# Performance work log

Measured on AMD Instinct MI355X. Metric: run time of the kernel, lower is better.

The kernel has to match this reference:

```python
import jax, jax.numpy as jnp
import numpy as np

B, N, L, D = 4, 32, 64, 512      # batch, num_nodes, his_len, input_dim
H, O = 1024, 512                  # expert hidden, output_dim
E, S, TOP_K = 16, 3, 2            # independent experts, shared experts, top-k


def setup_inputs() -> dict:
    key = jax.random.key(0)
    ks = jax.random.split(key, 12)
    sc = 0.02
    return {
        "feature_vectors": jax.random.normal(ks[0], (B, N, L, D), jnp.float32),
        "object_types": jax.random.uniform(ks[1], (B, N, L, S, 1), jnp.float32),
        "gating_w": jax.random.normal(ks[2], (D, E), jnp.float32) * sc,
        "gating_b": jnp.zeros((E,), jnp.float32),
        "sh_w1": jax.random.normal(ks[3], (S, D, H), jnp.float32) * sc,
        "sh_b1": jnp.zeros((S, H), jnp.float32),
        "sh_w2": jax.random.normal(ks[4], (S, H, O), jnp.float32) * sc,
        "sh_b2": jnp.zeros((S, O), jnp.float32),
        "ind_w1": jax.random.normal(ks[5], (E, D, H), jnp.float32) * sc,
        "ind_b1": jnp.zeros((E, H), jnp.float32),
        "ind_w2": jax.random.normal(ks[6], (E, H, O), jnp.float32) * sc,
        "ind_b2": jnp.zeros((E, O), jnp.float32),
    }


def reference(feature_vectors, object_types, gating_w, gating_b,
              sh_w1, sh_b1, sh_w2, sh_b2,
              ind_w1, ind_b1, ind_w2, ind_b2):
    b, n, l, d = feature_vectors.shape
    x = feature_vectors.reshape(-1, d)                       # [T, D]
    T = x.shape[0]

    # gating: softmax -> top-k -> renormalize selected weights
    gating = jax.nn.softmax(x @ gating_w + gating_b, axis=-1)  # [T, E]
    vals, idx = jax.lax.top_k(gating, TOP_K)                   # [T, K]
    w = vals / vals.sum(axis=-1, keepdims=True)                # [T, K]

    # shared experts: per-type FFN, weighted by object_types
    obj = object_types.reshape(-1, S, 1)                       # [T, S, 1]
    sh_h = jax.nn.relu(jnp.einsum('td,sdh->tsh', x, sh_w1) + sh_b1)
    sh_o = jnp.einsum('tsh,sho->tso', sh_h, sh_w2) + sh_b2     # [T, S, O]
    shared_out = (sh_o * obj).sum(axis=1)                      # [T, O]

    # independent experts: dense all-expert compute, combine via top-k weights
    # (equivalent to the bincount/mask dispatch loop: unselected experts get 0)
    ind_h = jax.nn.relu(jnp.einsum('td,edh->teh', x, ind_w1) + ind_b1)
    ind_o = jnp.einsum('teh,eho->teo', ind_h, ind_w2) + ind_b2  # [T, E, O]
    comb = jnp.zeros((T, gating_w.shape[1]), x.dtype)
    comb = comb.at[jnp.arange(T)[:, None], idx].add(w)          # [T, E] sparse weights
    ind_out = jnp.einsum('te,teo->to', comb, ind_o)             # [T, O]

    out = 0.5 * shared_out + 0.5 * ind_out
    return out.reshape(b, n, l, -1)
```

## Files before the change

kernel.cpp:

```cpp
#include <hip/hip_runtime.h>
#include <hip/hip_bf16.h>
#include <stdint.h>

#define T_TOK 8192
#define DIM   512
#define HID   1024
#define ODIM  512
#define NEXP  16
#define NSH   3

#define BM 128
#define BN 128
#define BK 64
#define MAXTILES 144
#define CAPSLOTS (MAXTILES * BM)

typedef __attribute__((ext_vector_type(8))) short s16x8;
typedef __attribute__((ext_vector_type(4))) float f32x4;

__device__ __forceinline__ uint16_t f2bf(float f) {
  union { float f; uint32_t u; } x; x.f = f;
  uint32_t r = x.u + 0x7FFFu + ((x.u >> 16) & 1u);
  return (uint16_t)(r >> 16);
}
__device__ __forceinline__ float bf2f(uint16_t u) {
  union { uint32_t u; float f; } x; x.u = ((uint32_t)u) << 16;
  return x.f;
}

__device__ __forceinline__ void async_copy16(const uint16_t* g, uint16_t* l) {
  __builtin_amdgcn_global_load_lds(
      (const __attribute__((address_space(1))) void*)g,
      (__attribute__((address_space(3))) void*)l, 16, 0, 0);
}

__global__ __launch_bounds__(256) void k_cvt_all(
    const float* __restrict__ shw1, const float* __restrict__ shw2,
    const float* __restrict__ iw1, const float* __restrict__ iw2,
    uint16_t* __restrict__ shw1T, uint16_t* __restrict__ shw2T,
    uint16_t* __restrict__ iw1T, uint16_t* __restrict__ iw2T) {
  __shared__ float tl[32][33];
  int id = blockIdx.x;
  const float* src; uint16_t* dst; int K, N, ldk; size_t dz;
  if (id < 1536)       { src = shw1; dst = shw1T; K = 512;  N = 1024; dz = (size_t)HID * DIM;  ldk = 512; }
  else if (id < 3072)  { src = shw2; dst = shw2T; K = 1024; N = 512;  dz = HID;                ldk = 3072; id -= 1536; }
  else if (id < 11264) { src = iw1;  dst = iw1T;  K = 512;  N = 1024; dz = (size_t)HID * DIM;  ldk = 512;  id -= 3072; }
  else                 { src = iw2;  dst = iw2T;  K = 1024; N = 512;  dz = (size_t)ODIM * HID; ldk = 1024; id -= 11264; }
  int z = id >> 9, tile = id & 511;
  int ntn = N >> 5;
  int n0 = (tile & (ntn - 1)) * 32, k0 = (tile / ntn) * 32;
  src += (size_t)z * K * N;
  dst += (size_t)z * dz;
  int tid = threadIdx.x, tx = tid & 31, ty = tid >> 5;
  int c4 = tx & 7, rr = ty + 8 * (tx >> 3);
  float4 v = *(const float4*)&src[(size_t)(k0 + rr) * N + n0 + c4 * 4];
  tl[rr][c4 * 4 + 0] = v.x; tl[rr][c4 * 4 + 1] = v.y;
  tl[rr][c4 * 4 + 2] = v.z; tl[rr][c4 * 4 + 3] = v.w;
  __syncthreads();
  int k4 = tx & 7, n = ty + 8 * (tx >> 3);
  ushort4 o;
  o.x = f2bf(tl[k4 * 4 + 0][n]); o.y = f2bf(tl[k4 * 4 + 1][n]);
  o.z = f2bf(tl[k4 * 4 + 2][n]); o.w = f2bf(tl[k4 * 4 + 3][n]);
  *(ushort4*)&dst[(size_t)(n0 + n) * ldk + k0 + k4 * 4] = o;
}

#define GTPB 16
__global__ __launch_bounds__(256) void k_gating(const float* __restrict__ x,
                                                const float* __restrict__ gw,
                                                const float* __restrict__ gb,
                                                uint16_t* __restrict__ xb,
                                                int* __restrict__ tok_top,
                                                float* __restrict__ wgt_top,
                                                int* __restrict__ cnt) {
  __shared__ float xs[GTPB][516];
  __shared__ float gws[NEXP][516];
  __shared__ int hist[NEXP];
  int tid = threadIdx.x;
  int tb = blockIdx.x * GTPB;
  if (tid < NEXP) hist[tid] = 0;
#pragma unroll
  for (int it = 0; it < 8; ++it) {
    int idx = (it * 256 + tid) * 4;
    float4 v = *(const float4*)&gw[idx];
    int d = idx >> 4, e0 = idx & 15;
    gws[e0 + 0][d] = v.x; gws[e0 + 1][d] = v.y;
    gws[e0 + 2][d] = v.z; gws[e0 + 3][d] = v.w;
  }
#pragma unroll
  for (int it = 0; it < 8; ++it) {
    int idx = it * 1024 + tid * 4;
    float4 v = *(const float4*)&x[(size_t)tb * DIM + idx];
    *(float4*)&xs[idx >> 9][idx & 511] = v;
  }
  __syncthreads();
#pragma unroll
  for (int it = 0; it < 4; ++it) {
    int idx = it * 2048 + tid * 8;
    int row = idx >> 9, col = idx & 511;
    float4 v0 = *(const float4*)&xs[row][col];
    float4 v1 = *(const float4*)&xs[row][col + 4];
    ushort4 o0, o1;
    o0.x = f2bf(v0.x); o0.y = f2bf(v0.y); o0.z = f2bf(v0.z); o0.w = f2bf(v0.w);
    o1.x = f2bf(v1.x); o1.y = f2bf(v1.y); o1.z = f2bf(v1.z); o1.w = f2bf(v1.w);
    *(ushort4*)&xb[(size_t)(tb + row) * DIM + col] = o0;
    *(ushort4*)&xb[(size_t)(tb + row) * DIM + col + 4] = o1;
  }
  int tok = tid >> 4, e = tid & 15;
  float acc = 0.f;
#pragma unroll 8
  for (int k = 0; k < DIM / 4; ++k) {
    float4 xv = *(const float4*)&xs[tok][k * 4];
    float4 gv = *(const float4*)&gws[e][k * 4];
    acc += xv.x * gv.x + xv.y * gv.y + xv.z * gv.z + xv.w * gv.w;
  }
  acc += gb[e];
  int lbase = (tid & 63) & 48;
  float best1 = -3.4e38f; int i1 = 0;
#pragma unroll
  for (int ee = 0; ee < NEXP; ++ee) {
    float v = __shfl(acc, lbase + ee, 64);
    if (v > best1) { best1 = v; i1 = ee; }
  }
  float best2 = -3.4e38f; int i2 = 0;
#pragma unroll
  for (int ee = 0; ee < NEXP; ++ee) {
    float v = __shfl(acc, lbase + ee, 64);
    if (ee != i1 && v > best2) { best2 = v; i2 = ee; }
  }
  if (e == 0) {
    int t = tb + tok;
    float w0 = 1.f / (1.f + expf(best2 - best1));
    tok_top[t * 2] = i1; tok_top[t * 2 + 1] = i2;
    wgt_top[t * 2] = w0; wgt_top[t * 2 + 1] = 1.f - w0;
    atomicAdd(&hist[i1], 1);
    atomicAdd(&hist[i2], 1);
  }
  __syncthreads();
  if (tid < NEXP && hist[tid]) atomicAdd(&cnt[tid], hist[tid]);
}

__global__ __launch_bounds__(256) void k_sched(const int* __restrict__ cnt,
                                               int* __restrict__ eoff,
                                               int* __restrict__ tdesc,
                                               int* __restrict__ ntl,
                                               int* __restrict__ rowtok,
                                               int* __restrict__ fill) {
  if (threadIdx.x == 0) {
    int o = 0, nt = 0;
    for (int e = 0; e < NEXP; ++e) {
      eoff[e] = o;
      int c = cnt[e];
      int t = (c + BM - 1) >> 7;
      for (int i = 0; i < t; ++i) { tdesc[nt * 2] = e; tdesc[nt * 2 + 1] = o + i * BM; ++nt; }
      o += t << 7;
      fill[e] = 0;
    }
    eoff[NEXP] = o;
    *ntl = nt;
  }
  for (int i = threadIdx.x; i < CAPSLOTS; i += 256) rowtok[i] = -1;
}

__global__ __launch_bounds__(256) void k_fill(const int* __restrict__ tok_top,
                                              const int* __restrict__ eoff,
                                              int* __restrict__ fill,
                                              int* __restrict__ rowtok,
                                              int* __restrict__ tok2slot) {
  int t = blockIdx.x * 256 + threadIdx.x;
  if (t >= T_TOK) return;
#pragma unroll
  for (int k = 0; k < 2; ++k) {
    int e = tok_top[t * 2 + k];
    int p = atomicAdd(&fill[e], 1);
    int slot = eoff[e] + p;
    rowtok[slot] = t;
    tok2slot[t * 2 + k] = slot;
  }
}

__device__ __forceinline__ void gemm_core(
    const uint16_t* a0, const uint16_t* a1, const uint16_t* a2, const uint16_t* a3,
    const uint16_t* b0, const uint16_t* b1, const uint16_t* b2, const uint16_t* b3,
    int nsteps, uint16_t* As, uint16_t* Bs, int wlds,
    int tl, int th, int wr, int wc, f32x4 (&acc)[4][4]) {
  const int sw = (tl & 7) << 3;
  for (int ks = 0; ks < nsteps; ++ks) {
    async_copy16(a0, As + wlds);           async_copy16(a1, As + wlds + 8 * BK);
    async_copy16(a2, As + wlds + 16 * BK); async_copy16(a3, As + wlds + 24 * BK);
    async_copy16(b0, Bs + wlds);           async_copy16(b1, Bs + wlds + 8 * BK);
    async_copy16(b2, Bs + wlds + 16 * BK); async_copy16(b3, Bs + wlds + 24 * BK);
    __syncthreads();
#pragma unroll
    for (int kk = 0; kk < 2; ++kk) {
      s16x8 af[4], bf[4];
#pragma unroll
      for (int i = 0; i < 4; ++i) {
        int eo = (kk * 32 + th * 8) ^ sw;
        af[i] = *(const s16x8*)&As[(wr * 64 + i * 16 + tl) * BK + eo];
        bf[i] = *(const s16x8*)&Bs[(wc * 64 + i * 16 + tl) * BK + eo];
      }
#pragma unroll
      for (int i = 0; i < 4; ++i)
#pragma unroll
        for (int j = 0; j < 4; ++j)
          acc[i][j] = __builtin_amdgcn_mfma_f32_16x16x32_bf16(af[i], bf[j], acc[i][j], 0, 0, 0);
    }
    __syncthreads();
    a0 += BK; a1 += BK; a2 += BK; a3 += BK;
    b0 += BK; b1 += BK; b2 += BK; b3 += BK;
  }
}

__global__ __launch_bounds__(256) void k_mega1(
    const uint16_t* __restrict__ xb, const uint16_t* __restrict__ shw1T,
    const float* __restrict__ shb1, const float* __restrict__ obj,
    uint16_t* __restrict__ hbuf,
    const int* __restrict__ tdesc, const int* __restrict__ ntl,
    const int* __restrict__ rowtok, const uint16_t* __restrict__ iw1T,
    const float* __restrict__ ib1, uint16_t* __restrict__ hind) {
  __shared__ uint16_t As[BM * BK], Bs[BN * BK];
  int id = blockIdx.x;
  int tid = threadIdx.x, lane = tid & 63, wid = tid >> 6;
  int wr = wid >> 1, wc = wid & 1, tl = lane & 15, th = lane >> 4;
  int lr = wid * 32 + (lane >> 3), koff = ((lane & 7) ^ (lane >> 3)) * 8;
  int wlds = wid * 32 * BK;
  f32x4 acc[4][4] = {};
  if (id < 1536) {
    int xcd = id & 7, g = id >> 3;
    int m0 = (xcd * 8 + g / 24) * BM;
    int n0 = (g % 24) * BN;
    const uint16_t* a0 = xb + (size_t)(m0 + lr) * DIM + koff;
    const uint16_t* b0 = shw1T + (size_t)(n0 + lr) * DIM + koff;
    gemm_core(a0, a0 + 8 * DIM, a0 + 16 * DIM, a0 + 24 * DIM,
              b0, b0 + 8 * DIM, b0 + 16 * DIM, b0 + 24 * DIM,
              DIM / BK, As, Bs, wlds, tl, th, wr, wc, acc);
#pragma unroll
    for (int i = 0; i < 4; ++i)
#pragma unroll
      for (int j = 0; j < 4; ++j) {
        int col = n0 + wc * 64 + j * 16 + tl;
        int s = col >> 10;
        float bv = shb1[col];
#pragma unroll
        for (int q = 0; q < 4; ++q) {
          int row = m0 + wr * 64 + i * 16 + th * 4 + q;
          float v = acc[i][j][q] + bv;
          float ow = 0.5f * obj[row * NSH + s];
          hbuf[(size_t)row * (NSH * HID) + col] = f2bf(ow * (v > 0.f ? v : 0.f));
        }
      }
  } else {
    int id2 = id - 1536;
    int xcd = id2 & 7, g = id2 >> 3;
    int t = xcd * 18 + (g >> 3);
    int n0 = (g & 7) * BN;
    if (t >= *ntl) return;
    int e = tdesc[t * 2], slot0 = tdesc[t * 2 + 1];
    const uint16_t* Bt = iw1T + (size_t)e * HID * DIM;
    const uint16_t* ap[4];
#pragma unroll
    for (int i = 0; i < 4; ++i) {
      int tk = rowtok[slot0 + lr + i * 8];
      if (tk < 0) tk = 0;
      ap[i] = xb + (size_t)tk * DIM + koff;
    }
    const uint16_t* b0 = Bt + (size_t)(n0 + lr) * DIM + koff;
    gemm_core(ap[0], ap[1], ap[2], ap[3],
              b0, b0 + 8 * DIM, b0 + 16 * DIM, b0 + 24 * DIM,
              DIM / BK, As, Bs, wlds, tl, th, wr, wc, acc);
#pragma unroll
    for (int i = 0; i < 4; ++i)
#pragma unroll
      for (int j = 0; j < 4; ++j) {
        int col = n0 + wc * 64 + j * 16 + tl;
        float bv = ib1[e * HID + col];
#pragma unroll
        for (int q = 0; q < 4; ++q) {
          int rowl = wr * 64 + i * 16 + th * 4 + q;
          float v = acc[i][j][q] + bv;
          hind[(size_t)(slot0 + rowl) * HID + col] = f2bf(v > 0.f ? v : 0.f);
        }
      }
  }
}

__global__ __launch_bounds__(256) void k_mega2(
    const uint16_t* __restrict__ hbuf, const uint16_t* __restrict__ shw2T,
    const float* __restrict__ shb2, const float* __restrict__ obj,
    float* __restrict__ outp,
    const int* __restrict__ tdesc, const int* __restrict__ ntl,
    const uint16_t* __restrict__ hind, const uint16_t* __restrict__ iw2T,
    const float* __restrict__ ib2,
    uint16_t* __restrict__ pind0, uint16_t* __restrict__ pind1) {
  __shared__ uint16_t As[BM * BK], Bs[BN * BK];
  int id = blockIdx.x;
  int tid = threadIdx.x, lane = tid & 63, wid = tid >> 6;
  int wr = wid >> 1, wc = wid & 1, tl = lane & 15, th = lane >> 4;
  int lr = wid * 32 + (lane >> 3), koff = ((lane & 7) ^ (lane >> 3)) * 8;
  int wlds = wid * 32 * BK;
  f32x4 acc[4][4] = {};
  if (id < 256) {
    const int K = NSH * HID;
    int xcd = id & 7, g = id >> 3;
    int m0 = (xcd * 8 + (g >> 2)) * BM;
    int n0 = (g & 3) * BN;
    const uint16_t* a0 = hbuf + (size_t)(m0 + lr) * K + koff;
    const uint16_t* b0 = shw2T + (size_t)(n0 + lr) * K + koff;
    gemm_core(a0, a0 + 8 * K, a0 + 16 * K, a0 + 24 * K,
              b0, b0 + 8 * K, b0 + 16 * K, b0 + 24 * K,
              K / BK, As, Bs, wlds, tl, th, wr, wc, acc);
#pragma unroll
    for (int i = 0; i < 4; ++i) {
      int rows[4]; float ob[4][NSH];
#pragma unroll
      for (int q = 0; q < 4; ++q) {
        rows[q] = m0 + wr * 64 + i * 16 + th * 4 + q;
#pragma unroll
        for (int s = 0; s < NSH; ++s) ob[q][s] = 0.5f * obj[rows[q] * NSH + s];
      }
#pragma unroll
      for (int j = 0; j < 4; ++j) {
        int col = n0 + wc * 64 + j * 16 + tl;
#pragma unroll
        for (int q = 0; q < 4; ++q) {
          float v = acc[i][j][q];
#pragma unroll
          for (int s = 0; s < NSH; ++s) v += ob[q][s] * shb2[s * ODIM + col];
          outp[(size_t)rows[q] * ODIM + col] = v;
        }
      }
    }
  } else {
    int id2 = id - 256;
    int xcd = id2 & 7, g = id2 >> 3;
    int t = xcd * 18 + (g >> 3);
    int inner = g & 7, n0 = (inner & 3) * BN, ksplit = inner >> 2;
    if (t >= *ntl) return;
    int e = tdesc[t * 2], slot0 = tdesc[t * 2 + 1];
    const uint16_t* a0 = hind + (size_t)(slot0 + lr) * HID + ksplit * 512 + koff;
    const uint16_t* b0 = iw2T + (size_t)e * ODIM * HID + (size_t)(n0 + lr) * HID +
                         ksplit * 512 + koff;
    gemm_core(a0, a0 + 8 * HID, a0 + 16 * HID, a0 + 24 * HID,
              b0, b0 + 8 * HID, b0 + 16 * HID, b0 + 24 * HID,
              512 / BK, As, Bs, wlds, tl, th, wr, wc, acc);
    uint16_t* pout = ksplit ? pind1 : pind0;
#pragma unroll
    for (int i = 0; i < 4; ++i)
#pragma unroll
      for (int j = 0; j < 4; ++j) {
        int col = n0 + wc * 64 + j * 16 + tl;
        float bv = ksplit ? 0.f : ib2[e * ODIM + col];
#pragma unroll
        for (int q = 0; q < 4; ++q) {
          int slot = slot0 + wr * 64 + i * 16 + th * 4 + q;
          pout[(size_t)slot * ODIM + col] = f2bf(acc[i][j][q] + bv);
        }
      }
  }
}

__global__ __launch_bounds__(256) void k_combine(float* __restrict__ outp,
                                                 const uint16_t* __restrict__ pind0,
                                                 const uint16_t* __restrict__ pind1,
                                                 const int* __restrict__ tok2slot,
                                                 const float* __restrict__ wgt_top) {
  int t = blockIdx.x * 4 + (threadIdx.x >> 6);
  int c = (threadIdx.x & 63) * 8;
  int s0 = tok2slot[t * 2], s1 = tok2slot[t * 2 + 1];
  float w0 = 0.5f * wgt_top[t * 2], w1 = 0.5f * wgt_top[t * 2 + 1];
  s16x8 p00 = *(const s16x8*)&pind0[(size_t)s0 * ODIM + c];
  s16x8 p01 = *(const s16x8*)&pind1[(size_t)s0 * ODIM + c];
  s16x8 p10 = *(const s16x8*)&pind0[(size_t)s1 * ODIM + c];
  s16x8 p11 = *(const s16x8*)&pind1[(size_t)s1 * ODIM + c];
  float* op = &outp[(size_t)t * ODIM + c];
  float4 o0 = *(float4*)op, o1 = *(float4*)(op + 4);
  float r[8];
#pragma unroll
  for (int j = 0; j < 8; ++j)
    r[j] = w0 * (bf2f((uint16_t)p00[j]) + bf2f((uint16_t)p01[j])) +
           w1 * (bf2f((uint16_t)p10[j]) + bf2f((uint16_t)p11[j]));
  o0.x += r[0]; o0.y += r[1]; o0.z += r[2]; o0.w += r[3];
  o1.x += r[4]; o1.y += r[5]; o1.z += r[6]; o1.w += r[7];
  *(float4*)op = o0; *(float4*)(op + 4) = o1;
}

extern "C" void kernel_launch(void* const* d_in, const int* in_sizes, int n_in,
                              void* d_out, int out_size, void* d_ws, size_t ws_size,
                              hipStream_t stream) {
  (void)in_sizes; (void)n_in; (void)out_size; (void)ws_size;
  const float* fv   = (const float*)d_in[0];
  const float* obj  = (const float*)d_in[1];
  const float* gw   = (const float*)d_in[2];
  const float* gb   = (const float*)d_in[3];
  const float* shw1 = (const float*)d_in[4];
  const float* shb1 = (const float*)d_in[5];
  const float* shw2 = (const float*)d_in[6];
  const float* shb2 = (const float*)d_in[7];
  const float* iw1  = (const float*)d_in[8];
  const float* ib1  = (const float*)d_in[9];
  const float* iw2  = (const float*)d_in[10];
  const float* ib2  = (const float*)d_in[11];
  float* outp = (float*)d_out;

  char* w = (char*)d_ws;
  size_t off = 0;
  auto alloc = [&](size_t bytes) {
    char* p = w + off;
    off = (off + bytes + 255) & ~(size_t)255;
    return p;
  };
  uint16_t* xb    = (uint16_t*)alloc((size_t)T_TOK * DIM * 2);
  uint16_t* hbuf  = (uint16_t*)alloc((size_t)T_TOK * NSH * HID * 2);
  uint16_t* hind  = (uint16_t*)alloc((size_t)CAPSLOTS * HID * 2);
  uint16_t* pind0 = (uint16_t*)alloc((size_t)CAPSLOTS * ODIM * 2);
  uint16_t* pind1 = (uint16_t*)alloc((size_t)CAPSLOTS * ODIM * 2);
  uint16_t* shw1T = (uint16_t*)alloc((size_t)NSH * HID * DIM * 2);
  uint16_t* shw2T = (uint16_t*)alloc((size_t)ODIM * NSH * HID * 2);
  uint16_t* iw1T  = (uint16_t*)alloc((size_t)NEXP * HID * DIM * 2);
  uint16_t* iw2T  = (uint16_t*)alloc((size_t)NEXP * ODIM * HID * 2);
  int*   tok_top  = (int*)alloc(T_TOK * 2 * 4);
  float* wgt_top  = (float*)alloc(T_TOK * 2 * 4);
  int*   tok2slot = (int*)alloc(T_TOK * 2 * 4);
  int*   rowtok   = (int*)alloc(CAPSLOTS * 4);
  int*   cnt      = (int*)alloc(64);
  int*   fill     = (int*)alloc(64);
  int*   eoff     = (int*)alloc((NEXP + 1) * 4);
  int*   tdesc    = (int*)alloc(MAXTILES * 2 * 4);
  int*   ntl      = (int*)alloc(4);

  hipMemsetAsync(cnt, 0, 64, stream);
  k_cvt_all<<<19456, 256, 0, stream>>>(shw1, shw2, iw1, iw2, shw1T, shw2T, iw1T, iw2T);
  k_gating<<<T_TOK / GTPB, 256, 0, stream>>>(fv, gw, gb, xb, tok_top, wgt_top, cnt);
  k_sched<<<1, 256, 0, stream>>>(cnt, eoff, tdesc, ntl, rowtok, fill);
  k_fill<<<T_TOK / 256, 256, 0, stream>>>(tok_top, eoff, fill, rowtok, tok2slot);

  k_mega1<<<1536 + 8 * MAXTILES, 256, 0, stream>>>(
      xb, shw1T, shb1, obj, hbuf, tdesc, ntl, rowtok, iw1T, ib1, hind);
  k_mega2<<<256 + 8 * MAXTILES, 256, 0, stream>>>(
      hbuf, shw2T, shb2, obj, outp, tdesc, ntl, hind, iw2T, ib2, pind0, pind1);
  k_combine<<<T_TOK / 4, 256, 0, stream>>>(outp, pind0, pind1, tok2slot, wgt_top);
}
```

Before: 237.8 us.

## Switch expert GEMMs to 256x256 tiles with double-buffered LDS pipeline

Replaces the 128x128 single-buffered GEMM core with a 512-thread, 256x256-tile kernel. It double-buffers A and B in LDS, interleaves async loads with MFMA phases and raises wave priority around the MFMA phases. Routing tiles grow to 256 rows, which changes the tile schedule and the capacity. The shared second GEMM is now split per shared expert and summed into the output with float atomics, so the output must be zeroed by an added memset. Larger tiles give more operand reuse per load, but they add padding waste on the routed experts, put atomic contention on the output and make the summation order nondeterministic.

New measurement: 268.5 us. +12.9%, slower.

```diff
diff --git a/kernel.cpp b/kernel.cpp
--- a/kernel.cpp
+++ b/kernel.cpp
@@ -9,11 +9,8 @@
 #define NEXP  16
 #define NSH   3
 
-#define BM 128
-#define BN 128
-#define BK 64
-#define MAXTILES 144
-#define CAPSLOTS (MAXTILES * BM)
+#define MAXTILES 80
+#define CAPSLOTS (MAXTILES * 256)
 
 typedef __attribute__((ext_vector_type(8))) short s16x8;
 typedef __attribute__((ext_vector_type(4))) float f32x4;
@@ -150,9 +147,9 @@
     for (int e = 0; e < NEXP; ++e) {
       eoff[e] = o;
       int c = cnt[e];
-      int t = (c + BM - 1) >> 7;
-      for (int i = 0; i < t; ++i) { tdesc[nt * 2] = e; tdesc[nt * 2 + 1] = o + i * BM; ++nt; }
-      o += t << 7;
+      int t = (c + 255) >> 8;
+      for (int i = 0; i < t; ++i) { tdesc[nt * 2] = e; tdesc[nt * 2 + 1] = o + i * 256; ++nt; }
+      o += t << 8;
       fill[e] = 0;
     }
     eoff[NEXP] = o;
@@ -178,113 +175,174 @@
   }
 }
 
-__device__ __forceinline__ void gemm_core(
-    const uint16_t* a0, const uint16_t* a1, const uint16_t* a2, const uint16_t* a3,
-    const uint16_t* b0, const uint16_t* b1, const uint16_t* b2, const uint16_t* b3,
-    int nsteps, uint16_t* As, uint16_t* Bs, int wlds,
-    int tl, int th, int wr, int wc, f32x4 (&acc)[4][4]) {
-  const int sw = (tl & 7) << 3;
-  for (int ks = 0; ks < nsteps; ++ks) {
-    async_copy16(a0, As + wlds);           async_copy16(a1, As + wlds + 8 * BK);
-    async_copy16(a2, As + wlds + 16 * BK); async_copy16(a3, As + wlds + 24 * BK);
-    async_copy16(b0, Bs + wlds);           async_copy16(b1, Bs + wlds + 8 * BK);
-    async_copy16(b2, Bs + wlds + 16 * BK); async_copy16(b3, Bs + wlds + 24 * BK);
-    __syncthreads();
-#pragma unroll
-    for (int kk = 0; kk < 2; ++kk) {
-      s16x8 af[4], bf[4];
-#pragma unroll
-      for (int i = 0; i < 4; ++i) {
-        int eo = (kk * 32 + th * 8) ^ sw;
-        af[i] = *(const s16x8*)&As[(wr * 64 + i * 16 + tl) * BK + eo];
-        bf[i] = *(const s16x8*)&Bs[(wc * 64 + i * 16 + tl) * BK + eo];
-      }
-#pragma unroll
-      for (int i = 0; i < 4; ++i)
-#pragma unroll
-        for (int j = 0; j < 4; ++j)
-          acc[i][j] = __builtin_amdgcn_mfma_f32_16x16x32_bf16(af[i], bf[j], acc[i][j], 0, 0, 0);
-    }
-    __syncthreads();
-    a0 += BK; a1 += BK; a2 += BK; a3 += BK;
-    b0 += BK; b1 += BK; b2 += BK; b3 += BK;
-  }
-}
-
-__global__ __launch_bounds__(256) void k_mega1(
+#define MFMA16(ACC, MB, NB, AARR, BARR)                                         \
+  _Pragma("unroll") for (int mf = 0; mf < 4; ++mf)                              \
+  _Pragma("unroll") for (int nf = 0; nf < 2; ++nf)                              \
+  _Pragma("unroll") for (int kk = 0; kk < 2; ++kk)                              \
+    ACC[(MB) + mf][(NB) + nf] = __builtin_amdgcn_mfma_f32_16x16x32_bf16(        \
+        AARR[mf][kk], BARR[nf][kk], ACC[(MB) + mf][(NB) + nf], 0, 0, 0);
+
+__device__ __forceinline__ void gemm256(
+    const uint16_t* as0, const uint16_t* as1, const uint16_t* as2, const uint16_t* as3,
+    const uint16_t* bs0, const uint16_t* bs1, const uint16_t* bs2, const uint16_t* bs3,
+    int NT, uint16_t* ldsA, uint16_t* ldsB,
+    int tid, int wr, int wc, int tl, int th, f32x4 (&acc)[8][4]) {
+  const int swx = (tl & 7) << 3;
+  const int th8 = th * 8;
+  const int rb0 = (wc & 1) * 64;
+  uint16_t* dA = ldsA + tid * 8;
+  uint16_t* dB = ldsB + tid * 8;
+  async_copy16(as0, dA);            async_copy16(as1, dA + 4096);
+  async_copy16(as2, dA + 8192);     async_copy16(as3, dA + 12288);
+  as0 += 64; as1 += 64; as2 += 64; as3 += 64;
+  async_copy16(bs0, dB);            async_copy16(bs1, dB + 4096);
+  async_copy16(bs2, dB + 8192);     async_copy16(bs3, dB + 12288);
+  bs0 += 64; bs1 += 64; bs2 += 64; bs3 += 64;
+  async_copy16(bs0, dB + 16384);    async_copy16(bs1, dB + 20480);
+  async_copy16(bs2, dB + 24576);    async_copy16(bs3, dB + 28672);
+  bs0 += 64; bs1 += 64; bs2 += 64; bs3 += 64;
+  asm volatile("s_waitcnt vmcnt(4)\ns_barrier" ::: "memory");
+
+  for (int t = 0; t < NT; ++t) {
+    const int b = t & 1;
+    const uint16_t* RA = ldsA + ((b * 2 + wr) << 13);
+    const uint16_t* RB = ldsB + ((b * 2 + (wc >> 1)) << 13);
+    uint16_t* SA = dA + (((b ^ 1) * 2) << 13);
+    uint16_t* SB = dB + ((b * 2) << 13);
+    const bool stA = (t + 1 < NT), stB = (t + 2 < NT);
+    s16x8 a[4][2], bq0[2][2], bq1[2][2];
+#pragma unroll
+    for (int mf = 0; mf < 4; ++mf)
+#pragma unroll
+      for (int kk = 0; kk < 2; ++kk)
+        a[mf][kk] = *(const s16x8*)&RA[((mf * 16 + tl) << 6) + ((kk * 32 + th8) ^ swx)];
+#pragma unroll
+    for (int nf = 0; nf < 2; ++nf)
+#pragma unroll
+      for (int kk = 0; kk < 2; ++kk)
+        bq0[nf][kk] = *(const s16x8*)&RB[((rb0 + nf * 16 + tl) << 6) + ((kk * 32 + th8) ^ swx)];
+    if (stA) { async_copy16(as0, SA); async_copy16(as1, SA + 4096); }
+    asm volatile("s_barrier" ::: "memory");
+    __builtin_amdgcn_s_setprio(1);
+    MFMA16(acc, 0, 0, a, bq0)
+    __builtin_amdgcn_s_setprio(0);
+    asm volatile("s_barrier" ::: "memory");
+#pragma unroll
+    for (int nf = 0; nf < 2; ++nf)
+#pragma unroll
+      for (int kk = 0; kk < 2; ++kk)
+        bq1[nf][kk] = *(const s16x8*)&RB[((rb0 + (nf + 2) * 16 + tl) << 6) + ((kk * 32 + th8) ^ swx)];
+    if (stA) { async_copy16(as2, SA + 8192); async_copy16(as3, SA + 12288); }
+    as0 += 64; as1 += 64; as2 += 64; as3 += 64;
+    asm volatile("s_barrier" ::: "memory");
+    __builtin_amdgcn_s_setprio(1);
+    MFMA16(acc, 0, 2, a, bq1)
+    __builtin_amdgcn_s_setprio(0);
+    asm volatile("s_barrier" ::: "memory");
+#pragma unroll
+    for (int mf = 0; mf < 4; ++mf)
+#pragma unroll
+      for (int kk = 0; kk < 2; ++kk)
+        a[mf][kk] = *(const s16x8*)&RA[(((mf + 4) * 16 + tl) << 6) + ((kk * 32 + th8) ^ swx)];
+    if (stB) { async_copy16(bs0, SB); async_copy16(bs1, SB + 4096); }
+    asm volatile("s_barrier" ::: "memory");
+    __builtin_amdgcn_s_setprio(1);
+    MFMA16(acc, 4, 0, a, bq0)
+    __builtin_amdgcn_s_setprio(0);
+    asm volatile("s_barrier" ::: "memory");
+    if (stB) { async_copy16(bs2, SB + 8192); async_copy16(bs3, SB + 12288); }
+    bs0 += 64; bs1 += 64; bs2 += 64; bs3 += 64;
+    asm volatile("s_barrier" ::: "memory");
+    __builtin_amdgcn_s_setprio(1);
+    MFMA16(acc, 4, 2, a, bq1)
+    __builtin_amdgcn_s_setprio(0);
+    if (stB)      asm volatile("s_waitcnt vmcnt(4)\ns_barrier" ::: "memory");
+    else if (stA) asm volatile("s_waitcnt vmcnt(0)\ns_barrier" ::: "memory");
+    else          asm volatile("s_barrier" ::: "memory");
+  }
+}
+
+__global__ __launch_bounds__(512, 2) void k_mega1(
     const uint16_t* __restrict__ xb, const uint16_t* __restrict__ shw1T,
     const float* __restrict__ shb1, const float* __restrict__ obj,
     uint16_t* __restrict__ hbuf,
     const int* __restrict__ tdesc, const int* __restrict__ ntl,
     const int* __restrict__ rowtok, const uint16_t* __restrict__ iw1T,
     const float* __restrict__ ib1, uint16_t* __restrict__ hind) {
-  __shared__ uint16_t As[BM * BK], Bs[BN * BK];
+  __shared__ uint16_t ldsA[2 * 2 * 8192];
+  __shared__ uint16_t ldsB[2 * 2 * 8192];
   int id = blockIdx.x;
   int tid = threadIdx.x, lane = tid & 63, wid = tid >> 6;
-  int wr = wid >> 1, wc = wid & 1, tl = lane & 15, th = lane >> 4;
-  int lr = wid * 32 + (lane >> 3), koff = ((lane & 7) ^ (lane >> 3)) * 8;
-  int wlds = wid * 32 * BK;
-  f32x4 acc[4][4] = {};
-  if (id < 1536) {
+  int wr = wid >> 2, wc = wid & 3, tl = lane & 15, th = lane >> 4;
+  int srow = tid >> 3;
+  int scol = ((tid & 7) * 8) ^ ((srow & 7) * 8);
+  f32x4 acc[8][4] = {};
+  if (id < 384) {
     int xcd = id & 7, g = id >> 3;
-    int m0 = (xcd * 8 + g / 24) * BM;
-    int n0 = (g % 24) * BN;
-    const uint16_t* a0 = xb + (size_t)(m0 + lr) * DIM + koff;
-    const uint16_t* b0 = shw1T + (size_t)(n0 + lr) * DIM + koff;
-    gemm_core(a0, a0 + 8 * DIM, a0 + 16 * DIM, a0 + 24 * DIM,
-              b0, b0 + 8 * DIM, b0 + 16 * DIM, b0 + 24 * DIM,
-              DIM / BK, As, Bs, wlds, tl, th, wr, wc, acc);
-#pragma unroll
-    for (int i = 0; i < 4; ++i)
-#pragma unroll
-      for (int j = 0; j < 4; ++j) {
-        int col = n0 + wc * 64 + j * 16 + tl;
-        int s = col >> 10;
+    int m0 = (xcd * 4 + g / 12) * 256;
+    int n0 = (g % 12) * 256;
+    const uint16_t* as[4]; const uint16_t* bs[4];
+#pragma unroll
+    for (int r = 0; r < 4; ++r) {
+      as[r] = xb + (size_t)(m0 + srow + r * 64) * DIM + scol;
+      bs[r] = shw1T + (size_t)(n0 + srow + r * 64) * DIM + scol;
+    }
+    gemm256(as[0], as[1], as[2], as[3], bs[0], bs[1], bs[2], bs[3],
+            DIM / 64, ldsA, ldsB, tid, wr, wc, tl, th, acc);
+    int s = (n0 + wc * 64) >> 10;
+#pragma unroll
+    for (int mf = 0; mf < 8; ++mf) {
+      int rows[4]; float ow[4];
+#pragma unroll
+      for (int q = 0; q < 4; ++q) {
+        rows[q] = m0 + wr * 128 + mf * 16 + th * 4 + q;
+        ow[q] = 0.5f * obj[rows[q] * NSH + s];
+      }
+#pragma unroll
+      for (int nf = 0; nf < 4; ++nf) {
+        int col = n0 + wc * 64 + nf * 16 + tl;
         float bv = shb1[col];
 #pragma unroll
         for (int q = 0; q < 4; ++q) {
-          int row = m0 + wr * 64 + i * 16 + th * 4 + q;
-          float v = acc[i][j][q] + bv;
-          float ow = 0.5f * obj[row * NSH + s];
-          hbuf[(size_t)row * (NSH * HID) + col] = f2bf(ow * (v > 0.f ? v : 0.f));
+          float v = acc[mf][nf][q] + bv;
+          hbuf[(size_t)rows[q] * (NSH * HID) + col] = f2bf(ow[q] * (v > 0.f ? v : 0.f));
         }
       }
+    }
   } else {
-    int id2 = id - 1536;
+    int id2 = id - 384;
     int xcd = id2 & 7, g = id2 >> 3;
-    int t = xcd * 18 + (g >> 3);
-    int n0 = (g & 7) * BN;
+    int t = xcd * 10 + (g >> 2);
+    int n0 = (g & 3) * 256;
     if (t >= *ntl) return;
     int e = tdesc[t * 2], slot0 = tdesc[t * 2 + 1];
-    const uint16_t* Bt = iw1T + (size_t)e * HID * DIM;
-    const uint16_t* ap[4];
-#pragma unroll
-    for (int i = 0; i < 4; ++i) {
-      int tk = rowtok[slot0 + lr + i * 8];
+    const uint16_t* as[4]; const uint16_t* bs[4];
+#pragma unroll
+    for (int r = 0; r < 4; ++r) {
+      int tk = rowtok[slot0 + srow + r * 64];
       if (tk < 0) tk = 0;
-      ap[i] = xb + (size_t)tk * DIM + koff;
-    }
-    const uint16_t* b0 = Bt + (size_t)(n0 + lr) * DIM + koff;
-    gemm_core(ap[0], ap[1], ap[2], ap[3],
-              b0, b0 + 8 * DIM, b0 + 16 * DIM, b0 + 24 * DIM,
-              DIM / BK, As, Bs, wlds, tl, th, wr, wc, acc);
-#pragma unroll
-    for (int i = 0; i < 4; ++i)
-#pragma unroll
-      for (int j = 0; j < 4; ++j) {
-        int col = n0 + wc * 64 + j * 16 + tl;
+      as[r] = xb + (size_t)tk * DIM + scol;
+      bs[r] = iw1T + (size_t)e * HID * DIM + (size_t)(n0 + srow + r * 64) * DIM + scol;
+    }
+    gemm256(as[0], as[1], as[2], as[3], bs[0], bs[1], bs[2], bs[3],
+            DIM / 64, ldsA, ldsB, tid, wr, wc, tl, th, acc);
+#pragma unroll
+    for (int mf = 0; mf < 8; ++mf)
+#pragma unroll
+      for (int nf = 0; nf < 4; ++nf) {
+        int col = n0 + wc * 64 + nf * 16 + tl;
         float bv = ib1[e * HID + col];
 #pragma unroll
         for (int q = 0; q < 4; ++q) {
-          int rowl = wr * 64 + i * 16 + th * 4 + q;
-          float v = acc[i][j][q] + bv;
-          hind[(size_t)(slot0 + rowl) * HID + col] = f2bf(v > 0.f ? v : 0.f);
+          int slot = slot0 + wr * 128 + mf * 16 + th * 4 + q;
+          float v = acc[mf][nf][q] + bv;
+          hind[(size_t)slot * HID + col] = f2bf(v > 0.f ? v : 0.f);
         }
       }
   }
 }
 
-__global__ __launch_bounds__(256) void k_mega2(
+__global__ __launch_bounds__(512, 2) void k_mega2(
     const uint16_t* __restrict__ hbuf, const uint16_t* __restrict__ shw2T,
     const float* __restrict__ shb2, const float* __restrict__ obj,
     float* __restrict__ outp,
@@ -292,68 +350,71 @@
     const uint16_t* __restrict__ hind, const uint16_t* __restrict__ iw2T,
     const float* __restrict__ ib2,
     uint16_t* __restrict__ pind0, uint16_t* __restrict__ pind1) {
-  __shared__ uint16_t As[BM * BK], Bs[BN * BK];
+  __shared__ uint16_t ldsA[2 * 2 * 8192];
+  __shared__ uint16_t ldsB[2 * 2 * 8192];
   int id = blockIdx.x;
   int tid = threadIdx.x, lane = tid & 63, wid = tid >> 6;
-  int wr = wid >> 1, wc = wid & 1, tl = lane & 15, th = lane >> 4;
-  int lr = wid * 32 + (lane >> 3), koff = ((lane & 7) ^ (lane >> 3)) * 8;
-  int wlds = wid * 32 * BK;
-  f32x4 acc[4][4] = {};
-  if (id < 256) {
+  int wr = wid >> 2, wc = wid & 3, tl = lane & 15, th = lane >> 4;
+  int srow = tid >> 3;
+  int scol = ((tid & 7) * 8) ^ ((srow & 7) * 8);
+  f32x4 acc[8][4] = {};
+  if (id < 192) {
     const int K = NSH * HID;
     int xcd = id & 7, g = id >> 3;
-    int m0 = (xcd * 8 + (g >> 2)) * BM;
-    int n0 = (g & 3) * BN;
-    const uint16_t* a0 = hbuf + (size_t)(m0 + lr) * K + koff;
-    const uint16_t* b0 = shw2T + (size_t)(n0 + lr) * K + koff;
-    gemm_core(a0, a0 + 8 * K, a0 + 16 * K, a0 + 24 * K,
-              b0, b0 + 8 * K, b0 + 16 * K, b0 + 24 * K,
-              K / BK, As, Bs, wlds, tl, th, wr, wc, acc);
-#pragma unroll
-    for (int i = 0; i < 4; ++i) {
-      int rows[4]; float ob[4][NSH];
+    int m0 = (xcd * 4 + g / 6) * 256;
+    int r = g % 6, s = r >> 1, n0 = (r & 1) * 256;
+    const uint16_t* as[4]; const uint16_t* bs[4];
+#pragma unroll
+    for (int rr = 0; rr < 4; ++rr) {
+      as[rr] = hbuf + (size_t)(m0 + srow + rr * 64) * K + s * HID + scol;
+      bs[rr] = shw2T + (size_t)(n0 + srow + rr * 64) * K + s * HID + scol;
+    }
+    gemm256(as[0], as[1], as[2], as[3], bs[0], bs[1], bs[2], bs[3],
+            HID / 64, ldsA, ldsB, tid, wr, wc, tl, th, acc);
+#pragma unroll
+    for (int mf = 0; mf < 8; ++mf) {
+      int rows[4]; float ow[4];
 #pragma unroll
       for (int q = 0; q < 4; ++q) {
-        rows[q] = m0 + wr * 64 + i * 16 + th * 4 + q;
-#pragma unroll
-        for (int s = 0; s < NSH; ++s) ob[q][s] = 0.5f * obj[rows[q] * NSH + s];
+        rows[q] = m0 + wr * 128 + mf * 16 + th * 4 + q;
+        ow[q] = 0.5f * obj[rows[q] * NSH + s];
       }
 #pragma unroll
-      for (int j = 0; j < 4; ++j) {
-        int col = n0 + wc * 64 + j * 16 + tl;
-#pragma unroll
-        for (int q = 0; q < 4; ++q) {
-          float v = acc[i][j][q];
-#pragma unroll
-          for (int s = 0; s < NSH; ++s) v += ob[q][s] * shb2[s * ODIM + col];
-          outp[(size_t)rows[q] * ODIM + col] = v;
-        }
+      for (int nf = 0; nf < 4; ++nf) {
+        int col = n0 + wc * 64 + nf * 16 + tl;
+        float bv = shb2[s * ODIM + col];
+#pragma unroll
+        for (int q = 0; q < 4; ++q)
+          atomicAdd(&outp[(size_t)rows[q] * ODIM + col], acc[mf][nf][q] + ow[q] * bv);
       }
     }
   } else {
-    int id2 = id - 256;
+    int id2 = id - 192;
     int xcd = id2 & 7, g = id2 >> 3;
-    int t = xcd * 18 + (g >> 3);
-    int inner = g & 7, n0 = (inner & 3) * BN, ksplit = inner >> 2;
+    int t = xcd * 10 + (g >> 2);
+    int inner = g & 3, n0 = (inner & 1) * 256, ksplit = inner >> 1;
     if (t >= *ntl) return;
     int e = tdesc[t * 2], slot0 = tdesc[t * 2 + 1];
-    const uint16_t* a0 = hind + (size_t)(slot0 + lr) * HID + ksplit * 512 + koff;
-    const uint16_t* b0 = iw2T + (size_t)e * ODIM * HID + (size_t)(n0 + lr) * HID +
-                         ksplit * 512 + koff;
-    gemm_core(a0, a0 + 8 * HID, a0 + 16 * HID, a0 + 24 * HID,
-              b0, b0 + 8 * HID, b0 + 16 * HID, b0 + 24 * HID,
-              512 / BK, As, Bs, wlds, tl, th, wr, wc, acc);
+    const uint16_t* as[4]; const uint16_t* bs[4];
+#pragma unroll
+    for (int rr = 0; rr < 4; ++rr) {
+      as[rr] = hind + (size_t)(slot0 + srow + rr * 64) * HID + ksplit * 512 + scol;
+      bs[rr] = iw2T + (size_t)e * ODIM * HID + (size_t)(n0 + srow + rr * 64) * HID +
+               ksplit * 512 + scol;
+    }
+    gemm256(as[0], as[1], as[2], as[3], bs[0], bs[1], bs[2], bs[3],
+            512 / 64, ldsA, ldsB, tid, wr, wc, tl, th, acc);
     uint16_t* pout = ksplit ? pind1 : pind0;
 #pragma unroll
-    for (int i = 0; i < 4; ++i)
-#pragma unroll
-      for (int j = 0; j < 4; ++j) {
-        int col = n0 + wc * 64 + j * 16 + tl;
+    for (int mf = 0; mf < 8; ++mf)
+#pragma unroll
+      for (int nf = 0; nf < 4; ++nf) {
+        int col = n0 + wc * 64 + nf * 16 + tl;
         float bv = ksplit ? 0.f : ib2[e * ODIM + col];
 #pragma unroll
         for (int q = 0; q < 4; ++q) {
-          int slot = slot0 + wr * 64 + i * 16 + th * 4 + q;
-          pout[(size_t)slot * ODIM + col] = f2bf(acc[i][j][q] + bv);
+          int slot = slot0 + wr * 128 + mf * 16 + th * 4 + q;
+          pout[(size_t)slot * ODIM + col] = f2bf(acc[mf][nf][q] + bv);
         }
       }
   }
@@ -387,7 +448,7 @@
 extern "C" void kernel_launch(void* const* d_in, const int* in_sizes, int n_in,
                               void* d_out, int out_size, void* d_ws, size_t ws_size,
                               hipStream_t stream) {
-  (void)in_sizes; (void)n_in; (void)out_size; (void)ws_size;
+  (void)in_sizes; (void)n_in; (void)ws_size;
   const float* fv   = (const float*)d_in[0];
   const float* obj  = (const float*)d_in[1];
   const float* gw   = (const float*)d_in[2];
@@ -429,14 +490,15 @@
   int*   ntl      = (int*)alloc(4);
 
   hipMemsetAsync(cnt, 0, 64, stream);
+  hipMemsetAsync(d_out, 0, (size_t)out_size * 4, stream);
   k_cvt_all<<<19456, 256, 0, stream>>>(shw1, shw2, iw1, iw2, shw1T, shw2T, iw1T, iw2T);
   k_gating<<<T_TOK / GTPB, 256, 0, stream>>>(fv, gw, gb, xb, tok_top, wgt_top, cnt);
   k_sched<<<1, 256, 0, stream>>>(cnt, eoff, tdesc, ntl, rowtok, fill);
   k_fill<<<T_TOK / 256, 256, 0, stream>>>(tok_top, eoff, fill, rowtok, tok2slot);
 
-  k_mega1<<<1536 + 8 * MAXTILES, 256, 0, stream>>>(
+  k_mega1<<<704, 512, 0, stream>>>(
       xb, shw1T, shb1, obj, hbuf, tdesc, ntl, rowtok, iw1T, ib1, hind);
-  k_mega2<<<256 + 8 * MAXTILES, 256, 0, stream>>>(
+  k_mega2<<<512, 512, 0, stream>>>(
       hbuf, shw2T, shb2, obj, outp, tdesc, ntl, hind, iw2T, ib2, pind0, pind1);
   k_combine<<<T_TOK / 4, 256, 0, stream>>>(outp, pind0, pind1, tok2slot, wgt_top);
 }
```

## Use 64x64 transpose tiles in weight conversion and drop split-K in expert GEMM2

Applied to the files above, without the earlier changes.

The weight fp32-to-bf16 transpose kernel now uses 64x64 tiles with several loads per thread and 16-byte stores, so it launches a quarter as many blocks. The independent-expert second GEMM no longer splits K into two halves. Each tile now runs the full K=1024 loop and writes a single partial buffer, which halves the partial-output writes and the combine reads. The cost is half as many blocks in the expert GEMM phase, so there is less parallelism and possibly worse load balance.

After: 228.2 us. 1.04x faster.

```diff
diff --git a/kernel.cpp b/kernel.cpp
--- a/kernel.cpp
+++ b/kernel.cpp
@@ -39,29 +39,37 @@
     const float* __restrict__ iw1, const float* __restrict__ iw2,
     uint16_t* __restrict__ shw1T, uint16_t* __restrict__ shw2T,
     uint16_t* __restrict__ iw1T, uint16_t* __restrict__ iw2T) {
-  __shared__ float tl[32][33];
+  __shared__ float tl[64][68];
   int id = blockIdx.x;
   const float* src; uint16_t* dst; int K, N, ldk; size_t dz;
-  if (id < 1536)       { src = shw1; dst = shw1T; K = 512;  N = 1024; dz = (size_t)HID * DIM;  ldk = 512; }
-  else if (id < 3072)  { src = shw2; dst = shw2T; K = 1024; N = 512;  dz = HID;                ldk = 3072; id -= 1536; }
-  else if (id < 11264) { src = iw1;  dst = iw1T;  K = 512;  N = 1024; dz = (size_t)HID * DIM;  ldk = 512;  id -= 3072; }
-  else                 { src = iw2;  dst = iw2T;  K = 1024; N = 512;  dz = (size_t)ODIM * HID; ldk = 1024; id -= 11264; }
-  int z = id >> 9, tile = id & 511;
-  int ntn = N >> 5;
-  int n0 = (tile & (ntn - 1)) * 32, k0 = (tile / ntn) * 32;
+  if (id < 384)       { src = shw1; dst = shw1T; K = 512;  N = 1024; dz = (size_t)HID * DIM;  ldk = 512; }
+  else if (id < 768)  { src = shw2; dst = shw2T; K = 1024; N = 512;  dz = HID;                ldk = 3072; id -= 384; }
+  else if (id < 2816) { src = iw1;  dst = iw1T;  K = 512;  N = 1024; dz = (size_t)HID * DIM;  ldk = 512;  id -= 768; }
+  else                { src = iw2;  dst = iw2T;  K = 1024; N = 512;  dz = (size_t)ODIM * HID; ldk = 1024; id -= 2816; }
+  int z = id >> 7, tile = id & 127;
+  int ntn = N >> 6;
+  int n0 = (tile & (ntn - 1)) * 64, k0 = (tile / ntn) * 64;
   src += (size_t)z * K * N;
   dst += (size_t)z * dz;
-  int tid = threadIdx.x, tx = tid & 31, ty = tid >> 5;
-  int c4 = tx & 7, rr = ty + 8 * (tx >> 3);
-  float4 v = *(const float4*)&src[(size_t)(k0 + rr) * N + n0 + c4 * 4];
-  tl[rr][c4 * 4 + 0] = v.x; tl[rr][c4 * 4 + 1] = v.y;
-  tl[rr][c4 * 4 + 2] = v.z; tl[rr][c4 * 4 + 3] = v.w;
+  int tid = threadIdx.x;
+  int lr = tid >> 4, lc = (tid & 15) * 4;
+#pragma unroll
+  for (int p = 0; p < 4; ++p) {
+    int row = lr + p * 16;
+    float4 v = *(const float4*)&src[(size_t)(k0 + row) * N + n0 + lc];
+    tl[row][lc + 0] = v.x; tl[row][lc + 1] = v.y;
+    tl[row][lc + 2] = v.z; tl[row][lc + 3] = v.w;
+  }
   __syncthreads();
-  int k4 = tx & 7, n = ty + 8 * (tx >> 3);
-  ushort4 o;
-  o.x = f2bf(tl[k4 * 4 + 0][n]); o.y = f2bf(tl[k4 * 4 + 1][n]);
-  o.z = f2bf(tl[k4 * 4 + 2][n]); o.w = f2bf(tl[k4 * 4 + 3][n]);
-  *(ushort4*)&dst[(size_t)(n0 + n) * ldk + k0 + k4 * 4] = o;
+  int nr = tid >> 3, kc = (tid & 7) * 8;
+#pragma unroll
+  for (int p = 0; p < 2; ++p) {
+    int n = nr + p * 32;
+    s16x8 o;
+#pragma unroll
+    for (int j = 0; j < 8; ++j) o[j] = (short)f2bf(tl[kc + j][n]);
+    *(s16x8*)&dst[(size_t)(n0 + n) * ldk + k0 + kc] = o;
+  }
 }
 
 #define GTPB 16
@@ -291,7 +299,7 @@
     const int* __restrict__ tdesc, const int* __restrict__ ntl,
     const uint16_t* __restrict__ hind, const uint16_t* __restrict__ iw2T,
     const float* __restrict__ ib2,
-    uint16_t* __restrict__ pind0, uint16_t* __restrict__ pind1) {
+    uint16_t* __restrict__ pind) {
   __shared__ uint16_t As[BM * BK], Bs[BN * BK];
   int id = blockIdx.x;
   int tid = threadIdx.x, lane = tid & 63, wid = tid >> 6;
@@ -333,52 +341,46 @@
   } else {
     int id2 = id - 256;
     int xcd = id2 & 7, g = id2 >> 3;
-    int t = xcd * 18 + (g >> 3);
-    int inner = g & 7, n0 = (inner & 3) * BN, ksplit = inner >> 2;
+    int t = xcd * 18 + (g >> 2);
+    int n0 = (g & 3) * BN;
     if (t >= *ntl) return;
     int e = tdesc[t * 2], slot0 = tdesc[t * 2 + 1];
-    const uint16_t* a0 = hind + (size_t)(slot0 + lr) * HID + ksplit * 512 + koff;
-    const uint16_t* b0 = iw2T + (size_t)e * ODIM * HID + (size_t)(n0 + lr) * HID +
-                         ksplit * 512 + koff;
+    const uint16_t* a0 = hind + (size_t)(slot0 + lr) * HID + koff;
+    const uint16_t* b0 = iw2T + (size_t)e * ODIM * HID + (size_t)(n0 + lr) * HID + koff;
     gemm_core(a0, a0 + 8 * HID, a0 + 16 * HID, a0 + 24 * HID,
               b0, b0 + 8 * HID, b0 + 16 * HID, b0 + 24 * HID,
-              512 / BK, As, Bs, wlds, tl, th, wr, wc, acc);
-    uint16_t* pout = ksplit ? pind1 : pind0;
+              HID / BK, As, Bs, wlds, tl, th, wr, wc, acc);
 #pragma unroll
     for (int i = 0; i < 4; ++i)
 #pragma unroll
       for (int j = 0; j < 4; ++j) {
         int col = n0 + wc * 64 + j * 16 + tl;
-        float bv = ksplit ? 0.f : ib2[e * ODIM + col];
+        float bv = ib2[e * ODIM + col];
 #pragma unroll
         for (int q = 0; q < 4; ++q) {
           int slot = slot0 + wr * 64 + i * 16 + th * 4 + q;
-          pout[(size_t)slot * ODIM + col] = f2bf(acc[i][j][q] + bv);
+          pind[(size_t)slot * ODIM + col] = f2bf(acc[i][j][q] + bv);
         }
       }
   }
 }
 
 __global__ __launch_bounds__(256) void k_combine(float* __restrict__ outp,
-                                                 const uint16_t* __restrict__ pind0,
-                                                 const uint16_t* __restrict__ pind1,
+                                                 const uint16_t* __restrict__ pind,
                                                  const int* __restrict__ tok2slot,
                                                  const float* __restrict__ wgt_top) {
   int t = blockIdx.x * 4 + (threadIdx.x >> 6);
   int c = (threadIdx.x & 63) * 8;
   int s0 = tok2slot[t * 2], s1 = tok2slot[t * 2 + 1];
   float w0 = 0.5f * wgt_top[t * 2], w1 = 0.5f * wgt_top[t * 2 + 1];
-  s16x8 p00 = *(const s16x8*)&pind0[(size_t)s0 * ODIM + c];
-  s16x8 p01 = *(const s16x8*)&pind1[(size_t)s0 * ODIM + c];
-  s16x8 p10 = *(const s16x8*)&pind0[(size_t)s1 * ODIM + c];
-  s16x8 p11 = *(const s16x8*)&pind1[(size_t)s1 * ODIM + c];
+  s16x8 p0 = *(const s16x8*)&pind[(size_t)s0 * ODIM + c];
+  s16x8 p1 = *(const s16x8*)&pind[(size_t)s1 * ODIM + c];
   float* op = &outp[(size_t)t * ODIM + c];
   float4 o0 = *(float4*)op, o1 = *(float4*)(op + 4);
   float r[8];
 #pragma unroll
   for (int j = 0; j < 8; ++j)
-    r[j] = w0 * (bf2f((uint16_t)p00[j]) + bf2f((uint16_t)p01[j])) +
-           w1 * (bf2f((uint16_t)p10[j]) + bf2f((uint16_t)p11[j]));
+    r[j] = w0 * bf2f((uint16_t)p0[j]) + w1 * bf2f((uint16_t)p1[j]);
   o0.x += r[0]; o0.y += r[1]; o0.z += r[2]; o0.w += r[3];
   o1.x += r[4]; o1.y += r[5]; o1.z += r[6]; o1.w += r[7];
   *(float4*)op = o0; *(float4*)(op + 4) = o1;
@@ -412,8 +414,7 @@
   uint16_t* xb    = (uint16_t*)alloc((size_t)T_TOK * DIM * 2);
   uint16_t* hbuf  = (uint16_t*)alloc((size_t)T_TOK * NSH * HID * 2);
   uint16_t* hind  = (uint16_t*)alloc((size_t)CAPSLOTS * HID * 2);
-  uint16_t* pind0 = (uint16_t*)alloc((size_t)CAPSLOTS * ODIM * 2);
-  uint16_t* pind1 = (uint16_t*)alloc((size_t)CAPSLOTS * ODIM * 2);
+  uint16_t* pind  = (uint16_t*)alloc((size_t)CAPSLOTS * ODIM * 2);
   uint16_t* shw1T = (uint16_t*)alloc((size_t)NSH * HID * DIM * 2);
   uint16_t* shw2T = (uint16_t*)alloc((size_t)ODIM * NSH * HID * 2);
   uint16_t* iw1T  = (uint16_t*)alloc((size_t)NEXP * HID * DIM * 2);
@@ -429,14 +430,14 @@
   int*   ntl      = (int*)alloc(4);
 
   hipMemsetAsync(cnt, 0, 64, stream);
-  k_cvt_all<<<19456, 256, 0, stream>>>(shw1, shw2, iw1, iw2, shw1T, shw2T, iw1T, iw2T);
+  k_cvt_all<<<4864, 256, 0, stream>>>(shw1, shw2, iw1, iw2, shw1T, shw2T, iw1T, iw2T);
   k_gating<<<T_TOK / GTPB, 256, 0, stream>>>(fv, gw, gb, xb, tok_top, wgt_top, cnt);
   k_sched<<<1, 256, 0, stream>>>(cnt, eoff, tdesc, ntl, rowtok, fill);
   k_fill<<<T_TOK / 256, 256, 0, stream>>>(tok_top, eoff, fill, rowtok, tok2slot);
 
   k_mega1<<<1536 + 8 * MAXTILES, 256, 0, stream>>>(
       xb, shw1T, shb1, obj, hbuf, tdesc, ntl, rowtok, iw1T, ib1, hind);
-  k_mega2<<<256 + 8 * MAXTILES, 256, 0, stream>>>(
-      hbuf, shw2T, shb2, obj, outp, tdesc, ntl, hind, iw2T, ib2, pind0, pind1);
-  k_combine<<<T_TOK / 4, 256, 0, stream>>>(outp, pind0, pind1, tok2slot, wgt_top);
-}
+  k_mega2<<<256 + 4 * MAXTILES, 256, 0, stream>>>(
+      hbuf, shw2T, shb2, obj, outp, tdesc, ntl, hind, iw2T, ib2, pind);
+  k_combine<<<T_TOK / 4, 256, 0, stream>>>(outp, pind, tok2slot, wgt_top);
+}
```
